# Optimization experiments

Hardware: AMD Instinct MI355X
Metric: run time of the kernel (lower is better)

## Reference

```python
import jax, jax.numpy as jnp
import numpy as np

B, N, D = 8, 2048, 512
DIM_ATTN, DIM_VAL = 512, 512


def setup_inputs() -> dict:
    key = jax.random.key(0)
    ks = jax.random.split(key, 7)
    s = 1.0 / np.sqrt(D)
    return {
        "x": jax.random.normal(ks[0], (B, N, D), dtype=jnp.float32),
        "Wq": jax.random.normal(ks[1], (D, DIM_ATTN), dtype=jnp.float32) * s,
        "bq": jnp.zeros((DIM_ATTN,), dtype=jnp.float32),
        "Wk": jax.random.normal(ks[2], (D, DIM_ATTN), dtype=jnp.float32) * s,
        "bk": jnp.zeros((DIM_ATTN,), dtype=jnp.float32),
        "Wv": jax.random.normal(ks[3], (D, DIM_VAL), dtype=jnp.float32) * s,
        "bv": jnp.zeros((DIM_VAL,), dtype=jnp.float32),
    }


def reference(x, Wq, bq, Wk, bk, Wv, bv):
    # relu-activated dense projections (Keras Dense with relu)
    Q = jax.nn.relu(jnp.einsum("bnd,de->bne", x, Wq) + bq)  # [B,N,dim_attn]
    K = jax.nn.relu(jnp.einsum("bnd,de->bne", x, Wk) + bk)  # [B,N,dim_attn]
    V = jax.nn.relu(jnp.einsum("bnd,de->bne", x, Wv) + bv)  # [B,N,dim_val]
    scale = 1.0 / jnp.sqrt(jnp.asarray(Q.shape[-1], dtype=jnp.float32))
    scores = jnp.einsum("bqe,bke->bqk", Q, K) * scale       # [B,N,N]
    attn = jax.nn.softmax(scores, axis=-1)
    return jnp.einsum("bqk,bkv->bqv", attn, V)               # [B,N,dim_val]
```

## Files before the change

kernel.cpp:

```cpp
#include <hip/hip_runtime.h>
#include <stdint.h>

typedef _Float16 f16;
typedef __attribute__((ext_vector_type(8))) _Float16 f16x8;
typedef __attribute__((ext_vector_type(4))) float f32x4;

#define QSCALE 0.0637587159f

__device__ __forceinline__ void gload16(const void* g, void* l) {
  __builtin_amdgcn_global_load_lds(
      (const __attribute__((address_space(1))) unsigned int*)(uintptr_t)g,
      (__attribute__((address_space(3))) unsigned int*)(uintptr_t)l,
      16, 0, 0);
}

__global__ __launch_bounds__(256) void k_cvt_x(const float* __restrict__ x,
                                               f16* __restrict__ xb) {
  const int i = (blockIdx.x * 256 + threadIdx.x) * 8;
  const float4 a = *(const float4*)(x + i);
  const float4 b = *(const float4*)(x + i + 4);
  f16x8 o;
  o[0] = (f16)a.x; o[1] = (f16)a.y; o[2] = (f16)a.z; o[3] = (f16)a.w;
  o[4] = (f16)b.x; o[5] = (f16)b.y; o[6] = (f16)b.z; o[7] = (f16)b.w;
  *(f16x8*)(xb + i) = o;
}

__global__ __launch_bounds__(256) void k_tw(const float* __restrict__ Wq,
                                            const float* __restrict__ Wk,
                                            const float* __restrict__ Wv,
                                            f16* __restrict__ Wqkt,
                                            f16* __restrict__ Wvt) {
  const int t = blockIdx.x * 256 + threadIdx.x;
  const int mat = t >> 16;
  const int rem = t & 65535;
  const int e = rem & 511;
  const int d4 = (rem >> 9) << 2;
  const float* W = (mat == 0) ? Wq : (mat == 1 ? Wk : Wv);
  f16* dst = (mat == 0) ? (Wqkt + e * 512)
           : (mat == 1 ? (Wqkt + (512 + e) * 512) : (Wvt + e * 512));
#pragma unroll
  for (int i = 0; i < 4; i++) dst[d4 + i] = (f16)W[(d4 + i) * 512 + e];
}

__device__ __forceinline__ void gemm_tile(const f16* __restrict__ Ag,
                                          const f16* __restrict__ Btg,
                                          f32x4 acc[4][4]) {
  __shared__ __align__(16) f16 As[128 * 64];
  __shared__ __align__(16) f16 Bs[128 * 64];
  const int lane = threadIdx.x & 63;
  const int w = threadIdx.x >> 6;
  const int wr = (w >> 1) * 64;
  const int wc = (w & 1) * 64;
#pragma unroll
  for (int i = 0; i < 4; i++)
#pragma unroll
    for (int j = 0; j < 4; j++) acc[i][j] = (f32x4){0.f, 0.f, 0.f, 0.f};

  for (int kt = 0; kt < 8; ++kt) {
#pragma unroll
    for (int i = 0; i < 4; i++) {
      const int r = w * 32 + i * 8 + (lane >> 3);
      const int src = kt * 64 + (((lane & 7) * 8) ^ ((r & 7) << 3));
      gload16(Ag + r * 512 + src, &As[(w * 32 + i * 8) * 64]);
      gload16(Btg + r * 512 + src, &Bs[(w * 32 + i * 8) * 64]);
    }
    __syncthreads();
#pragma unroll
    for (int ks = 0; ks < 2; ++ks) {
      f16x8 a[4], bfr[4];
#pragma unroll
      for (int i = 0; i < 4; i++) {
        const int row = wr + i * 16 + (lane & 15);
        a[i] = *(const f16x8*)&As[row * 64 +
                 ((ks * 32 + 8 * (lane >> 4)) ^ ((row & 7) << 3))];
      }
#pragma unroll
      for (int j = 0; j < 4; j++) {
        const int row = wc + j * 16 + (lane & 15);
        bfr[j] = *(const f16x8*)&Bs[row * 64 +
                 ((ks * 32 + 8 * (lane >> 4)) ^ ((row & 7) << 3))];
      }
#pragma unroll
      for (int i = 0; i < 4; i++)
#pragma unroll
        for (int j = 0; j < 4; j++)
          acc[i][j] = __builtin_amdgcn_mfma_f32_16x16x32_f16(a[i], bfr[j],
                                                             acc[i][j], 0, 0, 0);
    }
    __syncthreads();
  }
}

__global__ __launch_bounds__(256) void k_qk_proj(
    const f16* __restrict__ xb, const f16* __restrict__ Wqkt,
    const float* __restrict__ bq, const float* __restrict__ bk,
    f16* __restrict__ Q, f16* __restrict__ K) {
  const int rt = blockIdx.x, ct = blockIdx.y;
  f32x4 acc[4][4];
  gemm_tile(xb + rt * 128 * 512, Wqkt + ct * 128 * 512, acc);
  const int lane = threadIdx.x & 63;
  const int w = threadIdx.x >> 6;
  const int wr = (w >> 1) * 64, wc = (w & 1) * 64;
  const bool isQ = (ct < 4);
  const float* bias = isQ ? bq : bk;
  f16* dst = isQ ? Q : K;
  const int cb = (ct & 3) * 128;
  const float qs = isQ ? QSCALE : 1.0f;
#pragma unroll
  for (int j = 0; j < 4; j++) {
    const int col = cb + wc + j * 16 + (lane & 15);
    const float bb = bias[col];
#pragma unroll
    for (int i = 0; i < 4; i++) {
      const int nbase = rt * 128 + wr + i * 16 + 4 * (lane >> 4);
#pragma unroll
      for (int r = 0; r < 4; r++) {
        float v = fmaxf(acc[i][j][r] + bb, 0.f) * qs;
        dst[(nbase + r) * 512 + col] = (f16)v;
      }
    }
  }
}

__global__ __launch_bounds__(256) void k_v_proj(
    const f16* __restrict__ Wvt, const f16* __restrict__ xb,
    const float* __restrict__ bv, f16* __restrict__ Vt) {
  const int rt = blockIdx.x;
  const int ct = blockIdx.y;
  f32x4 acc[4][4];
  gemm_tile(Wvt + rt * 128 * 512, xb + ct * 128 * 512, acc);
  const int lane = threadIdx.x & 63;
  const int w = threadIdx.x >> 6;
  const int wr = (w >> 1) * 64, wc = (w & 1) * 64;
#pragma unroll
  for (int i = 0; i < 4; i++) {
    const int ebase = rt * 128 + wr + i * 16 + 4 * (lane >> 4);
#pragma unroll
    for (int j = 0; j < 4; j++) {
      const int n = ct * 128 + wc + j * 16 + (lane & 15);
      const int b = n >> 11, nb = n & 2047;
#pragma unroll
      for (int r = 0; r < 4; r++) {
        const int e = ebase + r;
        float v = fmaxf(acc[i][j][r] + bv[e], 0.f);
        Vt[(b * 512 + e) * 2048 + nb] = (f16)v;
      }
    }
  }
}

__global__ __launch_bounds__(256) void k_attn(
    const f16* __restrict__ Q, const f16* __restrict__ K,
    const f16* __restrict__ Vt, float* __restrict__ out) {
  __shared__ __align__(16) f16 Ks[64 * 512];
  __shared__ __align__(16) f16 Vs[512 * 64];
  __shared__ __align__(16) f16 Ps[4][16 * 72];
  const int b = blockIdx.x & 7;
  const int qb = blockIdx.x >> 3;
  const int lane = threadIdx.x & 63;
  const int w = threadIdx.x >> 6;
  const f16* Qg = Q + (b * 2048 + qb * 64) * 512;
  const f16* Kg = K + b * 2048 * 512;
  const f16* Vg = Vt + b * 512 * 2048;

#pragma unroll
  for (int i = 0; i < 16; i++) {
    const int r = w * 16 + i;
    const int src = (lane * 8) ^ ((r & 7) << 3);
    gload16(Qg + r * 512 + src, &Ks[r * 512]);
  }
  __syncthreads();
  f16x8 qf[16];
  {
    const int row = w * 16 + (lane & 15);
#pragma unroll
    for (int ks = 0; ks < 16; ++ks)
      qf[ks] = *(const f16x8*)&Ks[row * 512 +
               ((ks * 32 + 8 * (lane >> 4)) ^ ((row & 7) << 3))];
  }
  __syncthreads();

  f32x4 o[32];
#pragma unroll
  for (int i = 0; i < 32; i++) o[i] = (f32x4){0.f, 0.f, 0.f, 0.f};
  float m[4] = {-1e30f, -1e30f, -1e30f, -1e30f};
  float l[4] = {0.f, 0.f, 0.f, 0.f};

  for (int kt = 0; kt < 32; ++kt) {
#pragma unroll
    for (int i = 0; i < 16; i++) {
      const int r = w * 16 + i;
      const int src = (lane * 8) ^ ((r & 7) << 3);
      gload16(Kg + (kt * 64 + r) * 512 + src, &Ks[r * 512]);
    }
#pragma unroll
    for (int i = 0; i < 16; i++) {
      const int r = w * 128 + i * 8 + (lane >> 3);
      const int src = kt * 64 + (((lane & 7) * 8) ^ ((r & 7) << 3));
      gload16(Vg + r * 2048 + src, &Vs[(w * 128 + i * 8) * 64]);
    }
    __syncthreads();

    f32x4 s[4];
#pragma unroll
    for (int c = 0; c < 4; c++) s[c] = (f32x4){0.f, 0.f, 0.f, 0.f};
#pragma unroll
    for (int ks = 0; ks < 16; ++ks) {
#pragma unroll
      for (int c = 0; c < 4; c++) {
        const int row = c * 16 + (lane & 15);
        const f16x8 kf = *(const f16x8*)&Ks[row * 512 +
                        ((ks * 32 + 8 * (lane >> 4)) ^ ((row & 7) << 3))];
        s[c] = __builtin_amdgcn_mfma_f32_16x16x32_f16(qf[ks], kf, s[c], 0, 0, 0);
      }
    }

    float sc[4];
#pragma unroll
    for (int r = 0; r < 4; r++) {
      float v = fmaxf(fmaxf(s[0][r], s[1][r]), fmaxf(s[2][r], s[3][r]));
      v = fmaxf(v, __shfl_xor(v, 1));
      v = fmaxf(v, __shfl_xor(v, 2));
      v = fmaxf(v, __shfl_xor(v, 4));
      v = fmaxf(v, __shfl_xor(v, 8));
      const float nm = fmaxf(m[r], v);
      sc[r] = exp2f(m[r] - nm);
      m[r] = nm;
      float rs = 0.f;
      const int prow = 4 * (lane >> 4) + r;
#pragma unroll
      for (int c = 0; c < 4; c++) {
        const float pv = exp2f(s[c][r] - nm);
        Ps[w][prow * 72 + c * 16 + (lane & 15)] = (f16)pv;
        rs += pv;
      }
      rs += __shfl_xor(rs, 1);
      rs += __shfl_xor(rs, 2);
      rs += __shfl_xor(rs, 4);
      rs += __shfl_xor(rs, 8);
      l[r] = l[r] * sc[r] + rs;
    }
    {
      const f32x4 scv = {sc[0], sc[1], sc[2], sc[3]};
#pragma unroll
      for (int i = 0; i < 32; i++) o[i] *= scv;
    }

    const f16x8 pf0 = *(const f16x8*)&Ps[w][(lane & 15) * 72 + 8 * (lane >> 4)];
    const f16x8 pf1 = *(const f16x8*)&Ps[w][(lane & 15) * 72 + 32 + 8 * (lane >> 4)];
#pragma unroll
    for (int dt = 0; dt < 32; ++dt) {
      const int row = dt * 16 + (lane & 15);
      const f16x8 v0 = *(const f16x8*)&Vs[row * 64 +
                      ((8 * (lane >> 4)) ^ ((row & 7) << 3))];
      const f16x8 v1 = *(const f16x8*)&Vs[row * 64 +
                      ((32 + 8 * (lane >> 4)) ^ ((row & 7) << 3))];
      o[dt] = __builtin_amdgcn_mfma_f32_16x16x32_f16(pf0, v0, o[dt], 0, 0, 0);
      o[dt] = __builtin_amdgcn_mfma_f32_16x16x32_f16(pf1, v1, o[dt], 0, 0, 0);
    }
    __syncthreads();
  }

  float rl[4];
#pragma unroll
  for (int r = 0; r < 4; r++) rl[r] = 1.0f / l[r];
  float* ob = out + ((b * 2048 + qb * 64 + w * 16 + 4 * (lane >> 4)) * 512) + (lane & 15);
#pragma unroll
  for (int dt = 0; dt < 32; ++dt)
#pragma unroll
    for (int r = 0; r < 4; r++)
      ob[r * 512 + dt * 16] = o[dt][r] * rl[r];
}

extern "C" void kernel_launch(void* const* d_in, const int* in_sizes, int n_in,
                              void* d_out, int out_size, void* d_ws, size_t ws_size,
                              hipStream_t stream) {
  const float* x  = (const float*)d_in[0];
  const float* Wq = (const float*)d_in[1];
  const float* bq = (const float*)d_in[2];
  const float* Wk = (const float*)d_in[3];
  const float* bk = (const float*)d_in[4];
  const float* Wv = (const float*)d_in[5];
  const float* bv = (const float*)d_in[6];
  float* out = (float*)d_out;
  char* ws = (char*)d_ws;

  f16* xb   = (f16*)(ws);
  f16* Wqkt = (f16*)(ws + 16777216);
  f16* Wvt  = (f16*)(ws + 16777216 + 1048576);
  f16* Qb   = (f16*)(ws + 18350080);
  f16* Kb   = (f16*)(ws + 18350080 + 16777216);
  f16* Vtb  = (f16*)(ws + 18350080 + 2 * 16777216);

  hipLaunchKernelGGL(k_cvt_x, dim3(4096), dim3(256), 0, stream, x, xb);
  hipLaunchKernelGGL(k_tw, dim3(768), dim3(256), 0, stream, Wq, Wk, Wv, Wqkt, Wvt);
  hipLaunchKernelGGL(k_qk_proj, dim3(128, 8), dim3(256), 0, stream, xb, Wqkt, bq, bk, Qb, Kb);
  hipLaunchKernelGGL(k_v_proj, dim3(4, 128), dim3(256), 0, stream, Wvt, xb, bv, Vtb);
  hipLaunchKernelGGL(k_attn, dim3(256), dim3(256), 0, stream, Qb, Kb, Vtb, out);
}
```

Baseline: 355.6 us.

## Double-buffer K/V tiles in LDS with halved key tile for load overlap

The attention kernel's K/V tile size drops from 64 to 32 keys and two LDS buffers are used, so the next tile's global-to-LDS loads are issued before computing on the current one. V gets a new 32-wide swizzle layout and the per-tile MFMA and softmax loops shrink accordingly. This hides global load latency behind compute. In exchange the online-softmax rescale and the barrier now run twice as often, and LDS use stays near its limit.

```diff
diff --git a/kernel.cpp b/kernel.cpp
--- a/kernel.cpp
+++ b/kernel.cpp
@@ -152,9 +152,7 @@
 __global__ __launch_bounds__(256) void k_attn(
     const f16* __restrict__ Q, const f16* __restrict__ K,
     const f16* __restrict__ Vt, float* __restrict__ out) {
-  __shared__ __align__(16) f16 Ks[64 * 512];
-  __shared__ __align__(16) f16 Vs[512 * 64];
-  __shared__ __align__(16) f16 Ps[4][16 * 72];
+  __shared__ __align__(16) f16 smem[70144];
   const int b = blockIdx.x & 7;
   const int qb = blockIdx.x >> 3;
   const int lane = threadIdx.x & 63;
@@ -162,12 +160,13 @@
   const f16* Qg = Q + (b * 2048 + qb * 64) * 512;
   const f16* Kg = K + b * 2048 * 512;
   const f16* Vg = Vt + b * 512 * 2048;
+  f16* const Ps = smem + 65536;
 
 #pragma unroll
   for (int i = 0; i < 16; i++) {
     const int r = w * 16 + i;
     const int src = (lane * 8) ^ ((r & 7) << 3);
-    gload16(Qg + r * 512 + src, &Ks[r * 512]);
+    gload16(Qg + r * 512 + src, &smem[r * 512]);
   }
   __syncthreads();
   f16x8 qf[16];
@@ -175,8 +174,21 @@
     const int row = w * 16 + (lane & 15);
 #pragma unroll
     for (int ks = 0; ks < 16; ++ks)
-      qf[ks] = *(const f16x8*)&Ks[row * 512 +
+      qf[ks] = *(const f16x8*)&smem[row * 512 +
                ((ks * 32 + 8 * (lane >> 4)) ^ ((row & 7) << 3))];
+  }
+  __syncthreads();
+
+#pragma unroll
+  for (int i = 0; i < 8; i++) {
+    const int r = w * 8 + i;
+    gload16(Kg + r * 512 + ((lane * 8) ^ ((r & 7) << 3)), smem + r * 512);
+  }
+#pragma unroll
+  for (int i = 0; i < 8; i++) {
+    const int row = w * 128 + i * 16 + (lane >> 2);
+    const int col = (8 * (lane & 3)) ^ (8 * ((row >> 1) & 3));
+    gload16(Vg + row * 2048 + col, smem + 32768 + (w * 128 + i * 16) * 32);
   }
   __syncthreads();
 
@@ -185,29 +197,36 @@
   for (int i = 0; i < 32; i++) o[i] = (f32x4){0.f, 0.f, 0.f, 0.f};
   float m[4] = {-1e30f, -1e30f, -1e30f, -1e30f};
   float l[4] = {0.f, 0.f, 0.f, 0.f};
-
-  for (int kt = 0; kt < 32; ++kt) {
-#pragma unroll
-    for (int i = 0; i < 16; i++) {
-      const int r = w * 16 + i;
-      const int src = (lane * 8) ^ ((r & 7) << 3);
-      gload16(Kg + (kt * 64 + r) * 512 + src, &Ks[r * 512]);
-    }
-#pragma unroll
-    for (int i = 0; i < 16; i++) {
-      const int r = w * 128 + i * 8 + (lane >> 3);
-      const int src = kt * 64 + (((lane & 7) * 8) ^ ((r & 7) << 3));
-      gload16(Vg + r * 2048 + src, &Vs[(w * 128 + i * 8) * 64]);
-    }
-    __syncthreads();
-
-    f32x4 s[4];
-#pragma unroll
-    for (int c = 0; c < 4; c++) s[c] = (f32x4){0.f, 0.f, 0.f, 0.f};
+  int cur = 0;
+
+  for (int kt = 0; kt < 64; ++kt) {
+    if (kt < 63) {
+      const f16* Kgn = Kg + (kt + 1) * 32 * 512;
+      const f16* Vgn = Vg + (kt + 1) * 32;
+      f16* kd = smem + (cur ^ 1) * 16384;
+      f16* vd = smem + 32768 + (cur ^ 1) * 16384;
+#pragma unroll
+      for (int i = 0; i < 8; i++) {
+        const int r = w * 8 + i;
+        gload16(Kgn + r * 512 + ((lane * 8) ^ ((r & 7) << 3)), kd + r * 512);
+      }
+#pragma unroll
+      for (int i = 0; i < 8; i++) {
+        const int row = w * 128 + i * 16 + (lane >> 2);
+        const int col = (8 * (lane & 3)) ^ (8 * ((row >> 1) & 3));
+        gload16(Vgn + row * 2048 + col, vd + (w * 128 + i * 16) * 32);
+      }
+    }
+    const f16* Ks = smem + cur * 16384;
+    const f16* Vs = smem + 32768 + cur * 16384;
+
+    f32x4 s[2];
+#pragma unroll
+    for (int c = 0; c < 2; c++) s[c] = (f32x4){0.f, 0.f, 0.f, 0.f};
 #pragma unroll
     for (int ks = 0; ks < 16; ++ks) {
 #pragma unroll
-      for (int c = 0; c < 4; c++) {
+      for (int c = 0; c < 2; c++) {
         const int row = c * 16 + (lane & 15);
         const f16x8 kf = *(const f16x8*)&Ks[row * 512 +
                         ((ks * 32 + 8 * (lane >> 4)) ^ ((row & 7) << 3))];
@@ -218,7 +237,7 @@
     float sc[4];
 #pragma unroll
     for (int r = 0; r < 4; r++) {
-      float v = fmaxf(fmaxf(s[0][r], s[1][r]), fmaxf(s[2][r], s[3][r]));
+      float v = fmaxf(s[0][r], s[1][r]);
       v = fmaxf(v, __shfl_xor(v, 1));
       v = fmaxf(v, __shfl_xor(v, 2));
       v = fmaxf(v, __shfl_xor(v, 4));
@@ -229,9 +248,9 @@
       float rs = 0.f;
       const int prow = 4 * (lane >> 4) + r;
 #pragma unroll
-      for (int c = 0; c < 4; c++) {
+      for (int c = 0; c < 2; c++) {
         const float pv = exp2f(s[c][r] - nm);
-        Ps[w][prow * 72 + c * 16 + (lane & 15)] = (f16)pv;
+        Ps[w * 1152 + prow * 72 + c * 16 + (lane & 15)] = (f16)pv;
         rs += pv;
       }
       rs += __shfl_xor(rs, 1);
@@ -246,19 +265,17 @@
       for (int i = 0; i < 32; i++) o[i] *= scv;
     }
 
-    const f16x8 pf0 = *(const f16x8*)&Ps[w][(lane & 15) * 72 + 8 * (lane >> 4)];
-    const f16x8 pf1 = *(const f16x8*)&Ps[w][(lane & 15) * 72 + 32 + 8 * (lane >> 4)];
+    const f16x8 pf = *(const f16x8*)&Ps[w * 1152 + (lane & 15) * 72 +
+                                        8 * (lane >> 4)];
 #pragma unroll
     for (int dt = 0; dt < 32; ++dt) {
       const int row = dt * 16 + (lane & 15);
-      const f16x8 v0 = *(const f16x8*)&Vs[row * 64 +
-                      ((8 * (lane >> 4)) ^ ((row & 7) << 3))];
-      const f16x8 v1 = *(const f16x8*)&Vs[row * 64 +
-                      ((32 + 8 * (lane >> 4)) ^ ((row & 7) << 3))];
-      o[dt] = __builtin_amdgcn_mfma_f32_16x16x32_f16(pf0, v0, o[dt], 0, 0, 0);
-      o[dt] = __builtin_amdgcn_mfma_f32_16x16x32_f16(pf1, v1, o[dt], 0, 0, 0);
+      const f16x8 v0 = *(const f16x8*)&Vs[row * 32 +
+                      ((8 * (lane >> 4)) ^ (8 * ((row >> 1) & 3)))];
+      o[dt] = __builtin_amdgcn_mfma_f32_16x16x32_f16(pf, v0, o[dt], 0, 0, 0);
     }
     __syncthreads();
+    cur ^= 1;
   }
 
   float rl[4];
```

Measured after the change: 328.4 us. 1.08x faster.
